# Kernel optimization log

Measured on AMD Instinct MI355X. Metric: run time of the kernel, lower is better.

## Reference

```python
import jax, jax.numpy as jnp
import numpy as np

N = 50000      # nodes
E = 800000     # edges (avg degree 16)
NE = 100000    # query edges
IN = 128; HID = 128; OUT = 128; FEAT = 2


def _linear_params(k, fan_in, fan_out):
    # torch.nn.Linear default init: U(-1/sqrt(fan_in), 1/sqrt(fan_in))
    s = 1.0 / np.sqrt(fan_in)
    k1, k2 = jax.random.split(k)
    W = jax.random.uniform(k1, (fan_in, fan_out), jnp.float32, -s, s)
    b = jax.random.uniform(k2, (fan_out,), jnp.float32, -s, s)
    return W, b


def setup_inputs() -> dict:
    key = jax.random.key(0)
    ks = jax.random.split(key, 9)
    inp = {}
    inp["x"] = jax.random.normal(ks[0], (N, IN), jnp.float32)
    inp["adj_t"] = jax.random.randint(ks[1], (2, E), 0, N)          # edge_index [2,E]
    inp["train_edges"] = jax.random.randint(ks[2], (NE, 2), 0, N)   # query edges
    # GCNConv stack params (lin weight + bias per layer)
    inp["W1"], inp["b1"] = _linear_params(ks[3], IN, HID)
    inp["W2"], inp["b2"] = _linear_params(ks[4], HID, HID)
    inp["W3"], inp["b3"] = _linear_params(ks[5], HID, OUT)
    # LinkPredictor MLP params
    inp["P1"], inp["pb1"] = _linear_params(ks[6], OUT, HID)
    inp["P2"], inp["pb2"] = _linear_params(ks[7], HID, HID)
    inp["P3"], inp["pb3"] = _linear_params(ks[8], HID, FEAT)
    return inp


def gcn_conv(x, edge_index, W, b):
    # GCNConv(normalize=False), edge_weight=None:
    #   h = x @ W; out[dst] += h[src]; out += bias
    h = x @ W                                    # [N, d_out]
    msg = h[edge_index[0]]                       # gather  [E, d_out]
    out = jax.ops.segment_sum(msg, edge_index[1], num_segments=x.shape[0])
    return out + b


def reference(x, adj_t, train_edges, W1, b1, W2, b2, W3, b3, P1, pb1, P2, pb2, P3, pb3):
    # GCN trunk (eval mode -> dropout is identity; dropout=0 anyway)
    h = jax.nn.relu(gcn_conv(x, adj_t, W1, b1))
    h = jax.nn.relu(gcn_conv(h, adj_t, W2, b2))
    emb = gcn_conv(h, adj_t, W3, b3)             # [N, OUT]
    # LinkPredictor on (src, dst) node-embedding pairs
    z = emb[train_edges[:, 0]] * emb[train_edges[:, 1]]   # [NE, OUT]
    z = jax.nn.relu(z @ P1 + pb1)
    z = jax.nn.relu(z @ P2 + pb2)
    z = z @ P3 + pb3                                       # [NE, FEAT]
    # F.normalize(p=2, dim=-1) with eps=1e-12
    z = z / jnp.maximum(jnp.linalg.norm(z, axis=-1, keepdims=True), 1e-12)
    pred = jax.nn.log_softmax(z, axis=-1)
    return pred[None]                                      # torch.unsqueeze(pred, 0)
```

## Files before the change

### kernel.cpp

```cpp
#include <hip/hip_runtime.h>
#include <math.h>

#define N_NODES 50000
#define N_EDGES 800000
#define N_QE    100000
#define D       128

typedef _Float16 half4 __attribute__((ext_vector_type(4)));
typedef short    short8 __attribute__((ext_vector_type(8)));
typedef float    f32x4 __attribute__((ext_vector_type(4)));

static __device__ inline short f2bf(float f) {
    unsigned u = __builtin_bit_cast(unsigned, f);
    u += 0x7FFFu + ((u >> 16) & 1u);
    return (short)(u >> 16);
}
static __device__ inline short f2h(float f) {
    return (short)__builtin_bit_cast(unsigned short, (_Float16)f);
}

static const size_t O_CNT = 0;
static const size_t O_OFF = 256u * 1024;
static const size_t O_CUR = 512u * 1024;
static const size_t O_BS  = 768u * 1024;
static const size_t O_SRC = 1024u * 1024;
static const size_t O_A   = 8u << 20;
static const size_t O_H   = O_A + 25600000u;
static const size_t O_T   = O_H + 12800000u;

__global__ void k_count(const int* __restrict__ dst, int* __restrict__ cnt) {
    int e = blockIdx.x * 256 + threadIdx.x;
    if (e < N_EDGES) atomicAdd(&cnt[dst[e]], 1);
}

__global__ __launch_bounds__(256)
void k_scan1(const int* __restrict__ cnt, int* __restrict__ off,
             int* __restrict__ bsum) {
    __shared__ int sh[256];
    const int t = threadIdx.x;
    const int i = blockIdx.x * 256 + t;
    int v = (i < N_NODES) ? cnt[i] : 0;
    sh[t] = v;
    __syncthreads();
    #pragma unroll
    for (int o = 1; o < 256; o <<= 1) {
        int u = (t >= o) ? sh[t - o] : 0;
        __syncthreads();
        sh[t] += u;
        __syncthreads();
    }
    if (i < N_NODES) off[i] = sh[t] - v;
    if (t == 255) bsum[blockIdx.x] = sh[255];
}

__global__ __launch_bounds__(256)
void k_scan2(int* __restrict__ bsum, int nblk) {
    __shared__ int sh[256];
    const int t = threadIdx.x;
    int v = (t < nblk) ? bsum[t] : 0;
    sh[t] = v;
    __syncthreads();
    #pragma unroll
    for (int o = 1; o < 256; o <<= 1) {
        int u = (t >= o) ? sh[t - o] : 0;
        __syncthreads();
        sh[t] += u;
        __syncthreads();
    }
    if (t < nblk) bsum[t] = sh[t] - v;
}

__global__ __launch_bounds__(256)
void k_scan3(int* __restrict__ off, const int* __restrict__ bsum,
             int* __restrict__ cur) {
    const int i = blockIdx.x * 256 + threadIdx.x;
    if (i < N_NODES) {
        int o = off[i] + bsum[blockIdx.x];
        off[i] = o;
        cur[i] = o;
    }
    if (i == 0) off[N_NODES] = N_EDGES;
}

__global__ void k_scatter(const int* __restrict__ src, const int* __restrict__ dst,
                          int* __restrict__ cur, int* __restrict__ srcs) {
    int e = blockIdx.x * 256 + threadIdx.x;
    if (e < N_EDGES) {
        int p = atomicAdd(&cur[dst[e]], 1);
        srcs[p] = src[e];
    }
}

__global__ __launch_bounds__(256)
void k_t16all(const float* __restrict__ W1, const float* __restrict__ W2,
              const float* __restrict__ W3, const float* __restrict__ Q1,
              const float* __restrict__ Q2, short* __restrict__ T)
{
    int m = blockIdx.x >> 6;
    const float* S = (m == 0) ? W1 : (m == 1) ? W2 : (m == 2) ? W3
                   : (m == 3) ? Q1 : Q2;
    short* Dp = T + m * 16384;
    int idx = (blockIdx.x & 63) * 256 + threadIdx.x;
    int c = idx & 127, k = idx >> 7;
    Dp[c * 128 + k] = f2bf(S[k * 128 + c]);
}


__global__ __launch_bounds__(256)
void k_mm(const float* __restrict__ X, const short* __restrict__ WT,
          _Float16* __restrict__ Y, int rows)
{
    __shared__ __align__(16) short xs[64 * 128];
    const int tid = threadIdx.x;
    const int l   = tid & 63;
    const int w   = tid >> 6;
    const int g   = l >> 4;
    const int l15 = l & 15;
    const int row0 = blockIdx.x * 64;

    {
        int r = tid >> 2;
        int gr = row0 + r; if (gr >= rows) gr = rows - 1;
        const float* src = X + (size_t)gr * D;
        #pragma unroll
        for (int it = 0; it < 4; ++it) {
            int s = (tid & 3) + it * 4;
            float4 v0 = *(const float4*)(src + s * 8);
            float4 v1 = *(const float4*)(src + s * 8 + 4);
            short8 h;
            h[0] = f2bf(v0.x); h[1] = f2bf(v0.y);
            h[2] = f2bf(v0.z); h[3] = f2bf(v0.w);
            h[4] = f2bf(v1.x); h[5] = f2bf(v1.y);
            h[6] = f2bf(v1.z); h[7] = f2bf(v1.w);
            *(short8*)&xs[r * 128 + ((s ^ (r & 7)) * 8)] = h;
        }
    }

    short8 wf[2][4];
    #pragma unroll
    for (int tt = 0; tt < 2; ++tt) {
        int c = w * 32 + tt * 16 + l15;
        #pragma unroll
        for (int s = 0; s < 4; ++s)
            wf[tt][s] = *(const short8*)(WT + (size_t)c * 128 + s * 32 + g * 8);
    }

    __syncthreads();

    f32x4 acc[4][2];
    #pragma unroll
    for (int rt = 0; rt < 4; ++rt)
        #pragma unroll
        for (int tt = 0; tt < 2; ++tt)
            acc[rt][tt] = (f32x4){0.f, 0.f, 0.f, 0.f};

    #pragma unroll
    for (int rt = 0; rt < 4; ++rt) {
        const int r = rt * 16 + l15;
        short8 a[4];
        #pragma unroll
        for (int s = 0; s < 4; ++s) {
            int slot = (4 * s + g) ^ (r & 7);
            a[s] = *(const short8*)&xs[r * 128 + slot * 8];
        }
        #pragma unroll
        for (int tt = 0; tt < 2; ++tt)
            #pragma unroll
            for (int s = 0; s < 4; ++s)
                acc[rt][tt] = __builtin_amdgcn_mfma_f32_16x16x32_bf16(
                    a[s], wf[tt][s], acc[rt][tt], 0, 0, 0);
    }

    __syncthreads();

    #pragma unroll
    for (int rt = 0; rt < 4; ++rt)
        #pragma unroll
        for (int tt = 0; tt < 2; ++tt) {
            int c = w * 32 + tt * 16 + l15;
            #pragma unroll
            for (int i = 0; i < 4; ++i) {
                int row = rt * 16 + g * 4 + i;
                int slot = (c >> 3) ^ (row & 7);
                xs[row * 128 + slot * 8 + (c & 7)] = f2h(acc[rt][tt][i]);
            }
        }
    __syncthreads();

    {
        int r = tid >> 2;
        int gr = row0 + r;
        if (gr < rows) {
            short* dstp = (short*)(Y + (size_t)gr * D);
            #pragma unroll
            for (int it = 0; it < 4; ++it) {
                int s = (tid & 3) + it * 4;
                *(short8*)(dstp + s * 8) =
                    *(const short8*)&xs[r * 128 + ((s ^ (r & 7)) * 8)];
            }
        }
    }
}

template<bool RELU>
__global__ __launch_bounds__(256)
void k_agg(const _Float16* __restrict__ Hin, const int* __restrict__ off,
           const int* __restrict__ srcs, const float* __restrict__ bias,
           float* __restrict__ Hout)
{
    const int lane = threadIdx.x & 63;
    const int half = lane >> 5;
    const int q    = lane & 31;
    const int wv   = threadIdx.x >> 6;
    const int n    = blockIdx.x * 4 + wv;
    const int j0 = __builtin_amdgcn_readfirstlane(off[n]);
    const int j1 = __builtin_amdgcn_readfirstlane(off[n + 1]);

    float ax = 0.f, ay = 0.f, az = 0.f, aw = 0.f;
    int j = j0;

    for (; j + 16 <= j1; j += 16) {
        half4 v[8];
        #pragma unroll
        for (int k = 0; k < 8; ++k) {
            int sa = srcs[j + 2 * k];
            int sb = srcs[j + 2 * k + 1];
            int s = half ? sb : sa;
            v[k] = *(const half4*)(Hin + (size_t)s * D + q * 4);
        }
        #pragma unroll
        for (int k = 0; k < 8; ++k) {
            ax += (float)v[k].x; ay += (float)v[k].y;
            az += (float)v[k].z; aw += (float)v[k].w;
        }
    }
    for (; j + 4 <= j1; j += 4) {
        half4 v[2];
        #pragma unroll
        for (int k = 0; k < 2; ++k) {
            int sa = srcs[j + 2 * k];
            int sb = srcs[j + 2 * k + 1];
            int s = half ? sb : sa;
            v[k] = *(const half4*)(Hin + (size_t)s * D + q * 4);
        }
        #pragma unroll
        for (int k = 0; k < 2; ++k) {
            ax += (float)v[k].x; ay += (float)v[k].y;
            az += (float)v[k].z; aw += (float)v[k].w;
        }
    }
    for (; j + 2 <= j1; j += 2) {
        int sa = srcs[j];
        int sb = srcs[j + 1];
        int s = half ? sb : sa;
        half4 v = *(const half4*)(Hin + (size_t)s * D + q * 4);
        ax += (float)v.x; ay += (float)v.y; az += (float)v.z; aw += (float)v.w;
    }
    if (j < j1) {
        int s = srcs[j];
        if (!half) {
            half4 v = *(const half4*)(Hin + (size_t)s * D + q * 4);
            ax += (float)v.x; ay += (float)v.y; az += (float)v.z; aw += (float)v.w;
        }
    }

    ax += __shfl_xor(ax, 32, 64);
    ay += __shfl_xor(ay, 32, 64);
    az += __shfl_xor(az, 32, 64);
    aw += __shfl_xor(aw, 32, 64);

    if (!half) {
        const float4 bb = *(const float4*)(bias + q * 4);
        float4 o = make_float4(ax + bb.x, ay + bb.y, az + bb.z, aw + bb.w);
        if (RELU) {
            o.x = fmaxf(o.x, 0.f); o.y = fmaxf(o.y, 0.f);
            o.z = fmaxf(o.z, 0.f); o.w = fmaxf(o.w, 0.f);
        }
        *(float4*)(Hout + (size_t)n * D + q * 4) = o;
    }
}

__global__ __launch_bounds__(256)
void k_predm(const float* __restrict__ emb, const int* __restrict__ te,
             const short* __restrict__ P1T, const float* __restrict__ pb1,
             const short* __restrict__ P2T, const float* __restrict__ pb2,
             const float* __restrict__ P3, const float* __restrict__ pb3,
             float* __restrict__ out)
{
    __shared__ __align__(16) short xs[64 * 128];
    __shared__ float red[64][8];
    const int tid = threadIdx.x;
    const int l   = tid & 63;
    const int w   = tid >> 6;
    const int g   = l >> 4;
    const int l15 = l & 15;
    const int row0 = blockIdx.x * 64;

    {
        int r = tid >> 2;
        int e = row0 + r; if (e >= N_QE) e = N_QE - 1;
        const int2 ee = *(const int2*)(te + 2 * e);
        const float* sp = emb + (size_t)ee.x * D;
        const float* dp = emb + (size_t)ee.y * D;
        #pragma unroll
        for (int it = 0; it < 4; ++it) {
            int s = (tid & 3) + it * 4;
            float4 a0 = *(const float4*)(sp + s * 8);
            float4 a1 = *(const float4*)(sp + s * 8 + 4);
            float4 b0 = *(const float4*)(dp + s * 8);
            float4 b1 = *(const float4*)(dp + s * 8 + 4);
            short8 h;
            h[0] = f2bf(a0.x * b0.x); h[1] = f2bf(a0.y * b0.y);
            h[2] = f2bf(a0.z * b0.z); h[3] = f2bf(a0.w * b0.w);
            h[4] = f2bf(a1.x * b1.x); h[5] = f2bf(a1.y * b1.y);
            h[6] = f2bf(a1.z * b1.z); h[7] = f2bf(a1.w * b1.w);
            *(short8*)&xs[r * 128 + ((s ^ (r & 7)) * 8)] = h;
        }
    }
    __syncthreads();

    f32x4 acc[4][2];

    {
        short8 wf[2][4];
        #pragma unroll
        for (int tt = 0; tt < 2; ++tt) {
            int c = w * 32 + tt * 16 + l15;
            #pragma unroll
            for (int s = 0; s < 4; ++s)
                wf[tt][s] = *(const short8*)(P1T + (size_t)c * 128 + s * 32 + g * 8);
        }
        #pragma unroll
        for (int rt = 0; rt < 4; ++rt)
            #pragma unroll
            for (int tt = 0; tt < 2; ++tt)
                acc[rt][tt] = (f32x4){0.f, 0.f, 0.f, 0.f};

        #pragma unroll
        for (int rt = 0; rt < 4; ++rt) {
            const int r = rt * 16 + l15;
            short8 a[4];
            #pragma unroll
            for (int s = 0; s < 4; ++s) {
                int slot = (4 * s + g) ^ (r & 7);
                a[s] = *(const short8*)&xs[r * 128 + slot * 8];
            }
            #pragma unroll
            for (int tt = 0; tt < 2; ++tt)
                #pragma unroll
                for (int s = 0; s < 4; ++s)
                    acc[rt][tt] = __builtin_amdgcn_mfma_f32_16x16x32_bf16(
                        a[s], wf[tt][s], acc[rt][tt], 0, 0, 0);
        }

        float bv[2];
        #pragma unroll
        for (int tt = 0; tt < 2; ++tt) bv[tt] = pb1[w * 32 + tt * 16 + l15];

        __syncthreads();

        #pragma unroll
        for (int rt = 0; rt < 4; ++rt)
            #pragma unroll
            for (int tt = 0; tt < 2; ++tt) {
                int c = w * 32 + tt * 16 + l15;
                #pragma unroll
                for (int i = 0; i < 4; ++i) {
                    float v = fmaxf(acc[rt][tt][i] + bv[tt], 0.f);
                    int row = rt * 16 + g * 4 + i;
                    int slot = (c >> 3) ^ (row & 7);
                    xs[row * 128 + slot * 8 + (c & 7)] = f2bf(v);
                }
            }
        __syncthreads();
    }

    {
        short8 wf[2][4];
        #pragma unroll
        for (int tt = 0; tt < 2; ++tt) {
            int c = w * 32 + tt * 16 + l15;
            #pragma unroll
            for (int s = 0; s < 4; ++s)
                wf[tt][s] = *(const short8*)(P2T + (size_t)c * 128 + s * 32 + g * 8);
        }
        #pragma unroll
        for (int rt = 0; rt < 4; ++rt)
            #pragma unroll
            for (int tt = 0; tt < 2; ++tt)
                acc[rt][tt] = (f32x4){0.f, 0.f, 0.f, 0.f};

        #pragma unroll
        for (int rt = 0; rt < 4; ++rt) {
            const int r = rt * 16 + l15;
            short8 a[4];
            #pragma unroll
            for (int s = 0; s < 4; ++s) {
                int slot = (4 * s + g) ^ (r & 7);
                a[s] = *(const short8*)&xs[r * 128 + slot * 8];
            }
            #pragma unroll
            for (int tt = 0; tt < 2; ++tt)
                #pragma unroll
                for (int s = 0; s < 4; ++s)
                    acc[rt][tt] = __builtin_amdgcn_mfma_f32_16x16x32_bf16(
                        a[s], wf[tt][s], acc[rt][tt], 0, 0, 0);
        }
    }

    {
        float bv[2];
        float2 p3v[2];
        #pragma unroll
        for (int tt = 0; tt < 2; ++tt) {
            int c = w * 32 + tt * 16 + l15;
            bv[tt] = pb2[c];
            p3v[tt] = *(const float2*)(P3 + c * 2);
        }
        #pragma unroll
        for (int rt = 0; rt < 4; ++rt)
            #pragma unroll
            for (int i = 0; i < 4; ++i) {
                float z0 = fmaxf(acc[rt][0][i] + bv[0], 0.f);
                float z1 = fmaxf(acc[rt][1][i] + bv[1], 0.f);
                float p0 = z0 * p3v[0].x + z1 * p3v[1].x;
                float p1 = z0 * p3v[0].y + z1 * p3v[1].y;
                #pragma unroll
                for (int o = 1; o < 16; o <<= 1) {
                    p0 += __shfl_xor(p0, o, 64);
                    p1 += __shfl_xor(p1, o, 64);
                }
                if (l15 == 0) {
                    int row = rt * 16 + g * 4 + i;
                    red[row][w * 2]     = p0;
                    red[row][w * 2 + 1] = p1;
                }
            }
    }
    __syncthreads();

    if (tid < 64) {
        int gr = row0 + tid;
        if (gr < N_QE) {
            float p0 = red[tid][0] + red[tid][2] + red[tid][4] + red[tid][6] + pb3[0];
            float p1 = red[tid][1] + red[tid][3] + red[tid][5] + red[tid][7] + pb3[1];
            float nrm = fmaxf(sqrtf(p0 * p0 + p1 * p1), 1e-12f);
            p0 /= nrm; p1 /= nrm;
            float m = fmaxf(p0, p1);
            float lse = m + logf(expf(p0 - m) + expf(p1 - m));
            out[gr * 2]     = p0 - lse;
            out[gr * 2 + 1] = p1 - lse;
        }
    }
}

extern "C" void kernel_launch(void* const* d_in, const int* in_sizes, int n_in,
                              void* d_out, int out_size, void* d_ws, size_t ws_size,
                              hipStream_t stream)
{
    (void)in_sizes; (void)n_in; (void)out_size; (void)ws_size;
    const float* x   = (const float*)d_in[0];
    const int*   adj = (const int*)d_in[1];
    const int*   te  = (const int*)d_in[2];
    const float* W1  = (const float*)d_in[3];
    const float* b1  = (const float*)d_in[4];
    const float* W2  = (const float*)d_in[5];
    const float* b2  = (const float*)d_in[6];
    const float* W3  = (const float*)d_in[7];
    const float* b3  = (const float*)d_in[8];
    const float* P1  = (const float*)d_in[9];
    const float* pb1 = (const float*)d_in[10];
    const float* P2  = (const float*)d_in[11];
    const float* pb2 = (const float*)d_in[12];
    const float* P3  = (const float*)d_in[13];
    const float* pb3 = (const float*)d_in[14];
    float* out = (float*)d_out;

    char* ws = (char*)d_ws;
    int* cnt  = (int*)(ws + O_CNT);
    int* off  = (int*)(ws + O_OFF);
    int* cur  = (int*)(ws + O_CUR);
    int* bsum = (int*)(ws + O_BS);
    int* srcs = (int*)(ws + O_SRC);
    float*    A = (float*)(ws + O_A);
    _Float16* H = (_Float16*)(ws + O_H);
    short*    T = (short*)(ws + O_T);

    const int* esrc = adj;
    const int* edst = adj + N_EDGES;

    const int SBLK = (N_NODES + 255) / 256;

    k_t16all<<<320, 256, 0, stream>>>(W1, W2, W3, P1, P2, T);

    hipMemsetAsync(cnt, 0, N_NODES * sizeof(int), stream);
    k_count<<<N_EDGES / 256, 256, 0, stream>>>(edst, cnt);
    k_scan1<<<SBLK, 256, 0, stream>>>(cnt, off, bsum);
    k_scan2<<<1, 256, 0, stream>>>(bsum, SBLK);
    k_scan3<<<SBLK, 256, 0, stream>>>(off, bsum, cur);
    k_scatter<<<N_EDGES / 256, 256, 0, stream>>>(esrc, edst, cur, srcs);

    const int gN = (N_NODES + 63) / 64;
    const int gQ = (N_QE + 63) / 64;

    k_mm<<<gN, 256, 0, stream>>>(x, T,             H, N_NODES);
    k_agg<true><<<N_NODES / 4, 256, 0, stream>>>(H, off, srcs, b1, A);
    k_mm<<<gN, 256, 0, stream>>>(A, T + 16384,     H, N_NODES);
    k_agg<true><<<N_NODES / 4, 256, 0, stream>>>(H, off, srcs, b2, A);
    k_mm<<<gN, 256, 0, stream>>>(A, T + 2 * 16384, H, N_NODES);
    k_agg<false><<<N_NODES / 4, 256, 0, stream>>>(H, off, srcs, b3, A);

    k_predm<<<gQ, 256, 0, stream>>>(A, te, T + 3 * 16384, pb1,
                                    T + 4 * 16384, pb2, P3, pb3, out);
}
```

Baseline: 331.7 us.

## Store aggregated activations as fp16 and gather 16-byte rows in aggregation

The aggregation kernel now writes fp16 instead of fp32 output, so the following matmul and the link predictor read half the bytes. The aggregation kernel is also restructured so each wave processes four edges at once, with 16 lanes per edge each loading a half8. A two-step cross-lane shuffle then reduces the partial sums. This lowers memory traffic in three kernels and uses wider loads, in exchange for extra fp16 rounding of the intermediate activations and embeddings.

```diff
diff --git a/kernel.cpp b/kernel.cpp
--- a/kernel.cpp
+++ b/kernel.cpp
@@ -6,7 +6,7 @@
 #define N_QE    100000
 #define D       128
 
-typedef _Float16 half4 __attribute__((ext_vector_type(4)));
+typedef _Float16 half8 __attribute__((ext_vector_type(8)));
 typedef short    short8 __attribute__((ext_vector_type(8)));
 typedef float    f32x4 __attribute__((ext_vector_type(4)));
 
@@ -14,9 +14,6 @@
     unsigned u = __builtin_bit_cast(unsigned, f);
     u += 0x7FFFu + ((u >> 16) & 1u);
     return (short)(u >> 16);
-}
-static __device__ inline short f2h(float f) {
-    return (short)__builtin_bit_cast(unsigned short, (_Float16)f);
 }
 
 static const size_t O_CNT = 0;
@@ -24,8 +21,8 @@
 static const size_t O_CUR = 512u * 1024;
 static const size_t O_BS  = 768u * 1024;
 static const size_t O_SRC = 1024u * 1024;
-static const size_t O_A   = 8u << 20;
-static const size_t O_H   = O_A + 25600000u;
+static const size_t O_G   = 8u << 20;
+static const size_t O_H   = O_G + 12800000u;
 static const size_t O_T   = O_H + 12800000u;
 
 __global__ void k_count(const int* __restrict__ dst, int* __restrict__ cnt) {
@@ -106,8 +103,9 @@
 }
 
 
-__global__ __launch_bounds__(256)
-void k_mm(const float* __restrict__ X, const short* __restrict__ WT,
+template<typename XT>
+__global__ __launch_bounds__(256)
+void k_mm(const XT* __restrict__ X, const short* __restrict__ WT,
           _Float16* __restrict__ Y, int rows)
 {
     __shared__ __align__(16) short xs[64 * 128];
@@ -121,17 +119,23 @@
     {
         int r = tid >> 2;
         int gr = row0 + r; if (gr >= rows) gr = rows - 1;
-        const float* src = X + (size_t)gr * D;
+        const XT* src = X + (size_t)gr * D;
         #pragma unroll
         for (int it = 0; it < 4; ++it) {
             int s = (tid & 3) + it * 4;
-            float4 v0 = *(const float4*)(src + s * 8);
-            float4 v1 = *(const float4*)(src + s * 8 + 4);
             short8 h;
-            h[0] = f2bf(v0.x); h[1] = f2bf(v0.y);
-            h[2] = f2bf(v0.z); h[3] = f2bf(v0.w);
-            h[4] = f2bf(v1.x); h[5] = f2bf(v1.y);
-            h[6] = f2bf(v1.z); h[7] = f2bf(v1.w);
+            if constexpr (sizeof(XT) == 4) {
+                float4 v0 = *(const float4*)((const float*)src + s * 8);
+                float4 v1 = *(const float4*)((const float*)src + s * 8 + 4);
+                h[0] = f2bf(v0.x); h[1] = f2bf(v0.y);
+                h[2] = f2bf(v0.z); h[3] = f2bf(v0.w);
+                h[4] = f2bf(v1.x); h[5] = f2bf(v1.y);
+                h[6] = f2bf(v1.z); h[7] = f2bf(v1.w);
+            } else {
+                half8 v = *(const half8*)((const _Float16*)src + s * 8);
+                #pragma unroll
+                for (int c = 0; c < 8; ++c) h[c] = f2bf((float)v[c]);
+            }
             *(short8*)&xs[r * 128 + ((s ^ (r & 7)) * 8)] = h;
         }
     }
@@ -182,7 +186,8 @@
             for (int i = 0; i < 4; ++i) {
                 int row = rt * 16 + g * 4 + i;
                 int slot = (c >> 3) ^ (row & 7);
-                xs[row * 128 + slot * 8 + (c & 7)] = f2h(acc[rt][tt][i]);
+                xs[row * 128 + slot * 8 + (c & 7)] =
+                    (short)__builtin_bit_cast(unsigned short, (_Float16)acc[rt][tt][i]);
             }
         }
     __syncthreads();
@@ -206,82 +211,69 @@
 __global__ __launch_bounds__(256)
 void k_agg(const _Float16* __restrict__ Hin, const int* __restrict__ off,
            const int* __restrict__ srcs, const float* __restrict__ bias,
-           float* __restrict__ Hout)
+           _Float16* __restrict__ Hout)
 {
     const int lane = threadIdx.x & 63;
-    const int half = lane >> 5;
-    const int q    = lane & 31;
+    const int es   = lane >> 4;
+    const int q    = lane & 15;
     const int wv   = threadIdx.x >> 6;
     const int n    = blockIdx.x * 4 + wv;
     const int j0 = __builtin_amdgcn_readfirstlane(off[n]);
     const int j1 = __builtin_amdgcn_readfirstlane(off[n + 1]);
 
-    float ax = 0.f, ay = 0.f, az = 0.f, aw = 0.f;
+    float acc[8] = {};
     int j = j0;
 
     for (; j + 16 <= j1; j += 16) {
-        half4 v[8];
-        #pragma unroll
-        for (int k = 0; k < 8; ++k) {
-            int sa = srcs[j + 2 * k];
-            int sb = srcs[j + 2 * k + 1];
-            int s = half ? sb : sa;
-            v[k] = *(const half4*)(Hin + (size_t)s * D + q * 4);
-        }
-        #pragma unroll
-        for (int k = 0; k < 8; ++k) {
-            ax += (float)v[k].x; ay += (float)v[k].y;
-            az += (float)v[k].z; aw += (float)v[k].w;
-        }
+        half8 v[4];
+        #pragma unroll
+        for (int k = 0; k < 4; ++k) {
+            int s = srcs[j + 4 * k + es];
+            v[k] = *(const half8*)(Hin + (size_t)s * D + q * 8);
+        }
+        #pragma unroll
+        for (int k = 0; k < 4; ++k)
+            #pragma unroll
+            for (int c = 0; c < 8; ++c) acc[c] += (float)v[k][c];
     }
     for (; j + 4 <= j1; j += 4) {
-        half4 v[2];
-        #pragma unroll
-        for (int k = 0; k < 2; ++k) {
-            int sa = srcs[j + 2 * k];
-            int sb = srcs[j + 2 * k + 1];
-            int s = half ? sb : sa;
-            v[k] = *(const half4*)(Hin + (size_t)s * D + q * 4);
-        }
-        #pragma unroll
-        for (int k = 0; k < 2; ++k) {
-            ax += (float)v[k].x; ay += (float)v[k].y;
-            az += (float)v[k].z; aw += (float)v[k].w;
-        }
-    }
-    for (; j + 2 <= j1; j += 2) {
-        int sa = srcs[j];
-        int sb = srcs[j + 1];
-        int s = half ? sb : sa;
-        half4 v = *(const half4*)(Hin + (size_t)s * D + q * 4);
-        ax += (float)v.x; ay += (float)v.y; az += (float)v.z; aw += (float)v.w;
-    }
-    if (j < j1) {
-        int s = srcs[j];
-        if (!half) {
-            half4 v = *(const half4*)(Hin + (size_t)s * D + q * 4);
-            ax += (float)v.x; ay += (float)v.y; az += (float)v.z; aw += (float)v.w;
-        }
-    }
-
-    ax += __shfl_xor(ax, 32, 64);
-    ay += __shfl_xor(ay, 32, 64);
-    az += __shfl_xor(az, 32, 64);
-    aw += __shfl_xor(aw, 32, 64);
-
-    if (!half) {
-        const float4 bb = *(const float4*)(bias + q * 4);
-        float4 o = make_float4(ax + bb.x, ay + bb.y, az + bb.z, aw + bb.w);
-        if (RELU) {
-            o.x = fmaxf(o.x, 0.f); o.y = fmaxf(o.y, 0.f);
-            o.z = fmaxf(o.z, 0.f); o.w = fmaxf(o.w, 0.f);
-        }
-        *(float4*)(Hout + (size_t)n * D + q * 4) = o;
-    }
-}
-
-__global__ __launch_bounds__(256)
-void k_predm(const float* __restrict__ emb, const int* __restrict__ te,
+        int s = srcs[j + es];
+        half8 v = *(const half8*)(Hin + (size_t)s * D + q * 8);
+        #pragma unroll
+        for (int c = 0; c < 8; ++c) acc[c] += (float)v[c];
+    }
+    {
+        int rem = j1 - j;
+        if (rem > 0) {
+            int s = srcs[j + (es < rem ? es : rem - 1)];
+            half8 v = *(const half8*)(Hin + (size_t)s * D + q * 8);
+            if (es < rem) {
+                #pragma unroll
+                for (int c = 0; c < 8; ++c) acc[c] += (float)v[c];
+            }
+        }
+    }
+
+    #pragma unroll
+    for (int c = 0; c < 8; ++c) {
+        acc[c] += __shfl_xor(acc[c], 16, 64);
+        acc[c] += __shfl_xor(acc[c], 32, 64);
+    }
+
+    if (es == 0) {
+        half8 o;
+        #pragma unroll
+        for (int c = 0; c < 8; ++c) {
+            float t = acc[c] + bias[q * 8 + c];
+            if (RELU) t = fmaxf(t, 0.f);
+            o[c] = (_Float16)t;
+        }
+        *(half8*)(Hout + (size_t)n * D + q * 8) = o;
+    }
+}
+
+__global__ __launch_bounds__(256)
+void k_predm(const _Float16* __restrict__ emb, const int* __restrict__ te,
              const short* __restrict__ P1T, const float* __restrict__ pb1,
              const short* __restrict__ P2T, const float* __restrict__ pb2,
              const float* __restrict__ P3, const float* __restrict__ pb3,
@@ -300,20 +292,16 @@
         int r = tid >> 2;
         int e = row0 + r; if (e >= N_QE) e = N_QE - 1;
         const int2 ee = *(const int2*)(te + 2 * e);
-        const float* sp = emb + (size_t)ee.x * D;
-        const float* dp = emb + (size_t)ee.y * D;
+        const _Float16* sp = emb + (size_t)ee.x * D;
+        const _Float16* dp = emb + (size_t)ee.y * D;
         #pragma unroll
         for (int it = 0; it < 4; ++it) {
             int s = (tid & 3) + it * 4;
-            float4 a0 = *(const float4*)(sp + s * 8);
-            float4 a1 = *(const float4*)(sp + s * 8 + 4);
-            float4 b0 = *(const float4*)(dp + s * 8);
-            float4 b1 = *(const float4*)(dp + s * 8 + 4);
+            half8 a = *(const half8*)(sp + s * 8);
+            half8 b = *(const half8*)(dp + s * 8);
             short8 h;
-            h[0] = f2bf(a0.x * b0.x); h[1] = f2bf(a0.y * b0.y);
-            h[2] = f2bf(a0.z * b0.z); h[3] = f2bf(a0.w * b0.w);
-            h[4] = f2bf(a1.x * b1.x); h[5] = f2bf(a1.y * b1.y);
-            h[6] = f2bf(a1.z * b1.z); h[7] = f2bf(a1.w * b1.w);
+            #pragma unroll
+            for (int c = 0; c < 8; ++c) h[c] = f2bf((float)a[c] * (float)b[c]);
             *(short8*)&xs[r * 128 + ((s ^ (r & 7)) * 8)] = h;
         }
     }
@@ -482,7 +470,7 @@
     int* cur  = (int*)(ws + O_CUR);
     int* bsum = (int*)(ws + O_BS);
     int* srcs = (int*)(ws + O_SRC);
-    float*    A = (float*)(ws + O_A);
+    _Float16* G = (_Float16*)(ws + O_G);
     _Float16* H = (_Float16*)(ws + O_H);
     short*    T = (short*)(ws + O_T);
 
@@ -501,15 +489,15 @@
     k_scatter<<<N_EDGES / 256, 256, 0, stream>>>(esrc, edst, cur, srcs);
 
     const int gN = (N_NODES + 63) / 64;
+
+    k_mm<float><<<gN, 256, 0, stream>>>(x, T, H, N_NODES);
+    k_agg<true><<<N_NODES / 4, 256, 0, stream>>>(H, off, srcs, b1, G);
+    k_mm<_Float16><<<gN, 256, 0, stream>>>(G, T + 16384, H, N_NODES);
+    k_agg<true><<<N_NODES / 4, 256, 0, stream>>>(H, off, srcs, b2, G);
+    k_mm<_Float16><<<gN, 256, 0, stream>>>(G, T + 2 * 16384, H, N_NODES);
+    k_agg<false><<<N_NODES / 4, 256, 0, stream>>>(H, off, srcs, b3, G);
+
     const int gQ = (N_QE + 63) / 64;
-
-    k_mm<<<gN, 256, 0, stream>>>(x, T,             H, N_NODES);
-    k_agg<true><<<N_NODES / 4, 256, 0, stream>>>(H, off, srcs, b1, A);
-    k_mm<<<gN, 256, 0, stream>>>(A, T + 16384,     H, N_NODES);
-    k_agg<true><<<N_NODES / 4, 256, 0, stream>>>(H, off, srcs, b2, A);
-    k_mm<<<gN, 256, 0, stream>>>(A, T + 2 * 16384, H, N_NODES);
-    k_agg<false><<<N_NODES / 4, 256, 0, stream>>>(H, off, srcs, b3, A);
-
-    k_predm<<<gQ, 256, 0, stream>>>(A, te, T + 3 * 16384, pb1,
+    k_predm<<<gQ, 256, 0, stream>>>(G, te, T + 3 * 16384, pb1,
                                     T + 4 * 16384, pb2, P3, pb3, out);
 }
```

Measured after the change: 345.0 us. 4.0% more time.
